# Performance work log

Hardware: AMD Instinct MI355X
Metric: run time of the kernel (lower is better)

The kernel has to match this reference:

```python
import jax, jax.numpy as jnp
import numpy as np

M_POOL = 12500  # rows of the down_transform sparse matrix


def setup_inputs() -> dict:
    key = jax.random.key(0)
    ks = jax.random.split(key, 6)
    B, N, E, Cin, Cout, K, P = 4, 50000, 800000, 32, 64, 6, 50000
    x = jax.random.normal(ks[0], (B, N, Cin), jnp.float32)
    edge_index = jax.random.randint(ks[1], (2, E), 0, N, dtype=jnp.int64)
    pool_row = jax.random.randint(ks[2], (P,), 0, M_POOL, dtype=jnp.int64)
    pool_col = jax.random.randint(ks[3], (P,), 0, N, dtype=jnp.int64)
    pool_val = jax.random.uniform(ks[4], (P,), jnp.float32)
    # xavier_uniform over each [Cin, Cout] slice; bias zero-init (reset_parameters)
    limit = np.sqrt(6.0 / (Cin + Cout)).astype(np.float32)
    weight = jax.random.uniform(ks[5], (K, Cin, Cout), jnp.float32, -limit, limit)
    bias = jnp.zeros((Cout,), jnp.float32)
    return dict(x=x, edge_index=edge_index, pool_row=pool_row,
                pool_col=pool_col, pool_val=pool_val, weight=weight, bias=bias)


def _cheb_conv(x, edge_index, weight, bias):
    # x: [B, N, Cin]; weight: [K, Cin, Cout]
    N = x.shape[1]
    row, col = edge_index[0], edge_index[1]
    ones = jnp.ones(row.shape, x.dtype)
    deg = jax.ops.segment_sum(ones, row, num_segments=N)
    dis = jnp.where(deg > 0, jax.lax.rsqrt(jnp.where(deg > 0, deg, 1.0)), 0.0)
    # L_hat = 2L/lambda_max - I with lambda_max=2, sym norm -> diag 0, off-diag -d_i^-1/2 d_j^-1/2
    norm = -dis[row] * dis[col]  # [E]

    def prop(h):  # h: [B, N, C] -> L_hat @ h (gather, scale, scatter_add)
        msgs = h[:, col, :] * norm[None, :, None]  # [B, E, C]
        return jnp.zeros_like(h).at[:, row, :].add(msgs)

    Tx0 = x
    out = jnp.einsum('bnc,co->bno', Tx0, weight[0])
    Tx1 = prop(Tx0)
    out = out + jnp.einsum('bnc,co->bno', Tx1, weight[1])
    for k in range(2, weight.shape[0]):
        Tx2 = 2.0 * prop(Tx1) - Tx0
        out = out + jnp.einsum('bnc,co->bno', Tx2, weight[k])
        Tx0, Tx1 = Tx1, Tx2
    return out + bias


def reference(x, edge_index, pool_row, pool_col, pool_val, weight, bias):
    h = _cheb_conv(x, edge_index, weight, bias)  # single block (n_blocks=1)
    h = jax.nn.elu(h)
    # Pool: gather columns, scale by sparse values, scatter_add into rows
    B, _, C = h.shape
    gathered = h[:, pool_col, :] * pool_val[None, :, None]  # [B, P, C]
    out = jnp.zeros((B, M_POOL, C), h.dtype).at[:, pool_row, :].add(gathered)
    return out
```

## Files before the change

### kernel.cpp

```cpp
#include <hip/hip_runtime.h>
#include <hip/hip_fp16.h>
#include <cstdint>

#define N_NODES 50000
#define B_SZ 4
#define C_IN 32
#define C_OUT 64
#define K_CHEB 6
#define M_POOL 12500
#define NT_ROWS (N_NODES + M_POOL)
#define NS32 ((size_t)N_NODES * C_IN)
#define ZH ((size_t)N_NODES * C_OUT)
#define CN_CAP 2048

typedef _Float16 f16x8 __attribute__((ext_vector_type(8)));
typedef float f32x4 __attribute__((ext_vector_type(4)));
typedef unsigned short ushort_t;

__device__ __forceinline__ unsigned short f2h(float f) {
    union { _Float16 h; unsigned short u; } v;
    v.h = (_Float16)f;
    return v.u;
}

__device__ __forceinline__ float h2f(unsigned short u) {
    union { unsigned short u; _Float16 h; } v;
    v.u = u;
    return (float)v.h;
}

__device__ __forceinline__ __half2 u2h2(unsigned u) { return __builtin_bit_cast(__half2, u); }
__device__ __forceinline__ unsigned h22u(__half2 h) { return __builtin_bit_cast(unsigned, h); }

__global__ void zero_deg_kernel(int* __restrict__ deg) {
    int i = blockIdx.x * 256 + threadIdx.x;
    if (i < NT_ROWS) deg[i] = 0;
}

__global__ void deg_slot_kernel(const int* __restrict__ row, const int* __restrict__ prow,
                                int* __restrict__ deg, int* __restrict__ slot, int E, int P) {
    int base = (blockIdx.x * blockDim.x + threadIdx.x) * 4;
#pragma unroll
    for (int k = 0; k < 4; k++) {
        int e = base + k;
        if (e < E) slot[e] = atomicAdd(&deg[row[e]], 1);
        else if (e < E + P) slot[e] = atomicAdd(&deg[N_NODES + prow[e - E]], 1);
    }
}

__global__ void disdegp_kernel(const int* __restrict__ deg, float* __restrict__ dis,
                               int* __restrict__ degp) {
    int i = blockIdx.x * blockDim.x + threadIdx.x;
    if (i < N_NODES) {
        int d = deg[i];
        dis[i] = d > 0 ? rsqrtf((float)d) : 0.f;
        degp[i] = (d + 3) & ~3;
    } else if (i < NT_ROWS) {
        degp[i] = deg[i];
    }
}

__global__ void block_sum_kernel(const int* __restrict__ degp, int* __restrict__ bsum, int N) {
    __shared__ int sm[256];
    int i = blockIdx.x * 256 + threadIdx.x;
    sm[threadIdx.x] = (i < N) ? degp[i] : 0;
    __syncthreads();
    for (int s = 128; s > 0; s >>= 1) {
        if (threadIdx.x < s) sm[threadIdx.x] += sm[threadIdx.x + s];
        __syncthreads();
    }
    if (threadIdx.x == 0) bsum[blockIdx.x] = sm[0];
}

__global__ void scan_bsum_kernel(int* bsum, int nb, int* rowptr, int N) {
    if (blockIdx.x == 0 && threadIdx.x == 0) {
        int run = 0;
        for (int i = 0; i < nb; i++) { int v = bsum[i]; bsum[i] = run; run += v; }
        rowptr[N] = run;
    }
}

__global__ void rowptr_kernel(const int* __restrict__ degp, const int* __restrict__ bsum,
                              int* __restrict__ rowptr, int N) {
    __shared__ int sm[256];
    int i = blockIdx.x * 256 + threadIdx.x;
    sm[threadIdx.x] = (i < N) ? degp[i] : 0;
    __syncthreads();
    if (threadIdx.x == 0) {
        int run = bsum[blockIdx.x];
        for (int t = 0; t < 256; t++) { int v = sm[t]; sm[t] = run; run += v; }
    }
    __syncthreads();
    if (i < N) rowptr[i] = sm[threadIdx.x];
}

__global__ void pad_fill_kernel(const int* __restrict__ deg, const int* __restrict__ rowptr,
                                int2* __restrict__ cn) {
    int r = blockIdx.x * blockDim.x + threadIdx.x;
    if (r >= N_NODES) return;
    int p = rowptr[r] + deg[r];
    int p1 = rowptr[r + 1];
    for (; p < p1; ++p) cn[p] = make_int2(0, 0);
}

__global__ void place_all_kernel(const int* __restrict__ row, const int* __restrict__ col,
                                 const int* __restrict__ prow, const int* __restrict__ pcol,
                                 const float* __restrict__ pval, const float* __restrict__ dis,
                                 const int* __restrict__ rowptr, const int* __restrict__ slot,
                                 int2* __restrict__ cn, int E, int P) {
    int e = blockIdx.x * blockDim.x + threadIdx.x;
    if (e < E) {
        int r = row[e], c = col[e];
        float nm = -dis[r] * dis[c];
        unsigned h = f2h(nm);
        cn[rowptr[r] + slot[e]] = make_int2(c, (int)(h | (h << 16)));
    } else if (e < E + P) {
        int i = e - E;
        int r = N_NODES + prow[i];
        cn[rowptr[r] + slot[e]] = make_int2(pcol[i], __float_as_int(pval[i]));
    }
}

__global__ void cast_h_kernel(const float* __restrict__ in, unsigned int* __restrict__ out,
                              int n2) {
    int i = blockIdx.x * 256 + threadIdx.x;
    if (i < n2) {
        unsigned a = f2h(in[2 * i]), b = f2h(in[2 * i + 1]);
        out[i] = a | (b << 16);
    }
}

__global__ void prop_kernel(const ushort_t* __restrict__ hf, const ushort_t* __restrict__ p2f,
                            ushort_t* __restrict__ outf,
                            const int* __restrict__ rowptr, const int2* __restrict__ cn,
                            float alpha) {
    __shared__ int2 lcn[CN_CAP];
    int bid = blockIdx.x;
    int b = bid & 3;
    int grp = bid >> 2;
    int r0 = grp * 64;
    int rend = r0 + 64 > N_NODES ? N_NODES : r0 + 64;
    int pbase = rowptr[r0];
    int pend = rowptr[rend];
    int cnt = pend - pbase;
    bool use_lds = (cnt <= CN_CAP);
    if (use_lds) {
        for (int i = threadIdx.x; i < cnt; i += 256) lcn[i] = cn[pbase + i];
    }
    __syncthreads();

    int lr = threadIdx.x >> 2;
    int cs = threadIdx.x & 3;
    int r = r0 + lr;
    if (r >= N_NODES) return;
    const char* hb = (const char*)hf + (size_t)b * NS32 * 2;
    unsigned coff = (unsigned)cs * 16u;
    __half2 a0 = __float2half2_rn(0.f), a1 = a0, a2 = a0, a3 = a0;

    if (use_lds) {
        int p0 = rowptr[r] - pbase, p1 = rowptr[r + 1] - pbase;
        for (int p = p0; p < p1; p += 4) {
            int2 e0 = lcn[p], e1 = lcn[p + 1], e2 = lcn[p + 2], e3 = lcn[p + 3];
            uint4 v0 = *(const uint4*)(hb + (((unsigned)e0.x << 6) + coff));
            uint4 v1 = *(const uint4*)(hb + (((unsigned)e1.x << 6) + coff));
            uint4 v2 = *(const uint4*)(hb + (((unsigned)e2.x << 6) + coff));
            uint4 v3 = *(const uint4*)(hb + (((unsigned)e3.x << 6) + coff));
            __half2 n0 = u2h2((unsigned)e0.y), n1 = u2h2((unsigned)e1.y);
            __half2 n2 = u2h2((unsigned)e2.y), n3 = u2h2((unsigned)e3.y);
            a0 = __hfma2(u2h2(v0.x), n0, a0); a1 = __hfma2(u2h2(v0.y), n0, a1);
            a2 = __hfma2(u2h2(v0.z), n0, a2); a3 = __hfma2(u2h2(v0.w), n0, a3);
            a0 = __hfma2(u2h2(v1.x), n1, a0); a1 = __hfma2(u2h2(v1.y), n1, a1);
            a2 = __hfma2(u2h2(v1.z), n1, a2); a3 = __hfma2(u2h2(v1.w), n1, a3);
            a0 = __hfma2(u2h2(v2.x), n2, a0); a1 = __hfma2(u2h2(v2.y), n2, a1);
            a2 = __hfma2(u2h2(v2.z), n2, a2); a3 = __hfma2(u2h2(v2.w), n2, a3);
            a0 = __hfma2(u2h2(v3.x), n3, a0); a1 = __hfma2(u2h2(v3.y), n3, a1);
            a2 = __hfma2(u2h2(v3.z), n3, a2); a3 = __hfma2(u2h2(v3.w), n3, a3);
        }
    } else {
        int p0 = rowptr[r], p1 = rowptr[r + 1];
        for (int p = p0; p < p1; p += 4) {
            int2 e0 = cn[p], e1 = cn[p + 1], e2 = cn[p + 2], e3 = cn[p + 3];
            uint4 v0 = *(const uint4*)(hb + (((unsigned)e0.x << 6) + coff));
            uint4 v1 = *(const uint4*)(hb + (((unsigned)e1.x << 6) + coff));
            uint4 v2 = *(const uint4*)(hb + (((unsigned)e2.x << 6) + coff));
            uint4 v3 = *(const uint4*)(hb + (((unsigned)e3.x << 6) + coff));
            __half2 n0 = u2h2((unsigned)e0.y), n1 = u2h2((unsigned)e1.y);
            __half2 n2 = u2h2((unsigned)e2.y), n3 = u2h2((unsigned)e3.y);
            a0 = __hfma2(u2h2(v0.x), n0, a0); a1 = __hfma2(u2h2(v0.y), n0, a1);
            a2 = __hfma2(u2h2(v0.z), n0, a2); a3 = __hfma2(u2h2(v0.w), n0, a3);
            a0 = __hfma2(u2h2(v1.x), n1, a0); a1 = __hfma2(u2h2(v1.y), n1, a1);
            a2 = __hfma2(u2h2(v1.z), n1, a2); a3 = __hfma2(u2h2(v1.w), n1, a3);
            a0 = __hfma2(u2h2(v2.x), n2, a0); a1 = __hfma2(u2h2(v2.y), n2, a1);
            a2 = __hfma2(u2h2(v2.z), n2, a2); a3 = __hfma2(u2h2(v2.w), n2, a3);
            a0 = __hfma2(u2h2(v3.x), n3, a0); a1 = __hfma2(u2h2(v3.y), n3, a1);
            a2 = __hfma2(u2h2(v3.z), n3, a2); a3 = __hfma2(u2h2(v3.w), n3, a3);
        }
    }

    unsigned ooff = ((unsigned)r << 6) + coff;
    uint4 o;
    if (p2f) {
        __half2 al2 = __float2half2_rn(alpha);
        uint4 pv = *(const uint4*)((const char*)p2f + (size_t)b * NS32 * 2 + ooff);
        o.x = h22u(__hfma2(a0, al2, __hneg2(u2h2(pv.x))));
        o.y = h22u(__hfma2(a1, al2, __hneg2(u2h2(pv.y))));
        o.z = h22u(__hfma2(a2, al2, __hneg2(u2h2(pv.z))));
        o.w = h22u(__hfma2(a3, al2, __hneg2(u2h2(pv.w))));
    } else {
        o.x = h22u(a0); o.y = h22u(a1); o.z = h22u(a2); o.w = h22u(a3);
    }
    *(uint4*)((char*)outf + (size_t)b * NS32 * 2 + ooff) = o;
}

__global__ void packW_kernel(const float* __restrict__ W, ushort_t* __restrict__ Wp) {
    int i = blockIdx.x * 256 + threadIdx.x;
    if (i >= K_CHEB * 4 * 64 * 8) return;
    int j = i & 7;
    int lane = (i >> 3) & 63;
    int t = (i >> 9) & 3;
    int s = i >> 11;
    int k = (lane >> 4) * 8 + j;
    int col = t * 16 + (lane & 15);
    Wp[i] = f2h(W[((size_t)s * C_IN + k) * C_OUT + col]);
}

__global__ void gemm_mfma_kernel(const ushort_t* __restrict__ T0, const ushort_t* __restrict__ T1,
                                 const ushort_t* __restrict__ T2, const ushort_t* __restrict__ T3,
                                 const ushort_t* __restrict__ T4, const ushort_t* __restrict__ T5,
                                 const ushort_t* __restrict__ Wp,
                                 const float* __restrict__ bias, ushort_t* __restrict__ z) {
    int lane = threadIdx.x & 63;
    int wave = (blockIdx.x << 2) + (threadIdx.x >> 6);
    int r0 = wave << 4;
    int ga = r0 + (lane & 15);
    int koff = (lane >> 4) * 8;
    const ushort_t* Ts[6] = {T0, T1, T2, T3, T4, T5};

    f16x8 afr[6];
#pragma unroll
    for (int s = 0; s < 6; s++)
        afr[s] = *(const f16x8*)(Ts[s] + (size_t)ga * C_IN + koff);

    int orow = r0 + ((lane >> 4) << 2);
#pragma unroll
    for (int t = 0; t < 4; t++) {
        f32x4 acc = {0.f, 0.f, 0.f, 0.f};
#pragma unroll
        for (int s = 0; s < 6; s++) {
            f16x8 bfr = *(const f16x8*)(Wp + ((s * 4 + t) * 64 + lane) * 8);
            acc = __builtin_amdgcn_mfma_f32_16x16x32_f16(afr[s], bfr, acc, 0, 0, 0);
        }
        int col = (t << 4) + (lane & 15);
        float bv = bias[col];
#pragma unroll
        for (int rg = 0; rg < 4; rg++) {
            float v = acc[rg] + bv;
            z[(size_t)(orow + rg) * C_OUT + col] = f2h(v > 0.f ? v : (expf(v) - 1.f));
        }
    }
}

__global__ void pool_csr_kernel(const ushort_t* __restrict__ z, const int* __restrict__ rowptr,
                                const int2* __restrict__ cn, float* __restrict__ out) {
    int r = blockIdx.x * 8 + (threadIdx.x >> 5);
    int c2 = threadIdx.x & 31;
    if (r >= M_POOL) return;
    const char* zb = (const char*)z;
    unsigned coff = (unsigned)c2 << 2;
    float s00 = 0.f, s01 = 0.f, s10 = 0.f, s11 = 0.f;
    float s20 = 0.f, s21 = 0.f, s30 = 0.f, s31 = 0.f;
    int p0 = rowptr[N_NODES + r], p1 = rowptr[N_NODES + r + 1];
    for (int p = p0; p < p1; ++p) {
        int2 e = cn[p];
        float v = __int_as_float(e.y);
        unsigned off = ((unsigned)e.x << 7) + coff;
        unsigned u0 = *(const unsigned*)(zb + off);
        unsigned u1 = *(const unsigned*)(zb + ZH * 2 + off);
        unsigned u2 = *(const unsigned*)(zb + 2 * ZH * 2 + off);
        unsigned u3 = *(const unsigned*)(zb + 3 * ZH * 2 + off);
        s00 += h2f((ushort_t)u0) * v; s01 += h2f((ushort_t)(u0 >> 16)) * v;
        s10 += h2f((ushort_t)u1) * v; s11 += h2f((ushort_t)(u1 >> 16)) * v;
        s20 += h2f((ushort_t)u2) * v; s21 += h2f((ushort_t)(u2 >> 16)) * v;
        s30 += h2f((ushort_t)u3) * v; s31 += h2f((ushort_t)(u3 >> 16)) * v;
    }
    size_t idx = (size_t)r * C_OUT + 2 * c2;
    size_t bs = (size_t)M_POOL * C_OUT;
    *(float2*)&out[idx]          = make_float2(s00, s01);
    *(float2*)&out[idx + bs]     = make_float2(s10, s11);
    *(float2*)&out[idx + 2 * bs] = make_float2(s20, s21);
    *(float2*)&out[idx + 3 * bs] = make_float2(s30, s31);
}

extern "C" void kernel_launch(void* const* d_in, const int* in_sizes, int n_in,
                              void* d_out, int out_size, void* d_ws, size_t ws_size,
                              hipStream_t stream) {
    const float* x    = (const float*)d_in[0];
    const int*   ei   = (const int*)d_in[1];
    const int*   prow = (const int*)d_in[2];
    const int*   pcol = (const int*)d_in[3];
    const float* pval = (const float*)d_in[4];
    const float* W    = (const float*)d_in[5];
    const float* bias = (const float*)d_in[6];
    const int E = in_sizes[1] / 2;
    const int P = in_sizes[2];
    const int* row = ei;
    const int* col = ei + E;
    const int EP_MAX = E + 3 * N_NODES + P;

    char* ws = (char*)d_ws;
    size_t o = 0;
    auto alloc = [&](size_t bytes) -> char* {
        char* p = ws + o;
        o += (bytes + 255) & ~(size_t)255;
        return p;
    };
    int nb = (NT_ROWS + 255) / 256;
    int*   deg    = (int*)alloc((size_t)NT_ROWS * 4);
    int*   degp   = (int*)alloc((size_t)NT_ROWS * 4);
    float* dis    = (float*)alloc((size_t)N_NODES * 4);
    int*   rowptr = (int*)alloc((size_t)(NT_ROWS + 1) * 4);
    int*   slot   = (int*)alloc((size_t)(E + P) * 4);
    int*   bsum   = (int*)alloc((size_t)nb * 4);
    int2*  cn     = (int2*)alloc((size_t)EP_MAX * 8);
    ushort_t* Wp  = (ushort_t*)alloc((size_t)K_CHEB * 4 * 64 * 8 * 2);
    ushort_t* xh  = (ushort_t*)alloc((size_t)B_SZ * NS32 * 2);
    ushort_t* hA  = (ushort_t*)alloc((size_t)B_SZ * NS32 * 2);
    ushort_t* hB  = (ushort_t*)alloc((size_t)B_SZ * NS32 * 2);
    ushort_t* hC  = (ushort_t*)alloc((size_t)B_SZ * NS32 * 2);
    ushort_t* hD  = (ushort_t*)alloc((size_t)B_SZ * NS32 * 2);
    ushort_t* hE  = (ushort_t*)alloc((size_t)B_SZ * NS32 * 2);
    ushort_t* z   = (ushort_t*)alloc((size_t)B_SZ * ZH * 2);

    zero_deg_kernel<<<nb, 256, 0, stream>>>(deg);
    deg_slot_kernel<<<(E + P + 1023) / 1024, 256, 0, stream>>>(row, prow, deg, slot, E, P);
    disdegp_kernel<<<nb, 256, 0, stream>>>(deg, dis, degp);
    block_sum_kernel<<<nb, 256, 0, stream>>>(degp, bsum, NT_ROWS);
    scan_bsum_kernel<<<1, 64, 0, stream>>>(bsum, nb, rowptr, NT_ROWS);
    rowptr_kernel<<<nb, 256, 0, stream>>>(degp, bsum, rowptr, NT_ROWS);
    pad_fill_kernel<<<(N_NODES + 255) / 256, 256, 0, stream>>>(deg, rowptr, cn);
    place_all_kernel<<<(E + P + 255) / 256, 256, 0, stream>>>(row, col, prow, pcol, pval, dis,
                                                              rowptr, slot, cn, E, P);
    packW_kernel<<<(K_CHEB * 4 * 64 * 8 + 255) / 256, 256, 0, stream>>>(W, Wp);
    int n2 = (int)(B_SZ * NS32 / 2);
    cast_h_kernel<<<(n2 + 255) / 256, 256, 0, stream>>>(x, (unsigned int*)xh, n2);

    int prop_blocks = ((N_NODES + 63) / 64) * B_SZ;
    int gemm_blocks = (B_SZ * N_NODES) / 64;

    prop_kernel<<<prop_blocks, 256, 0, stream>>>(xh, nullptr, hA, rowptr, cn, 1.0f);
    prop_kernel<<<prop_blocks, 256, 0, stream>>>(hA, xh, hB, rowptr, cn, 2.0f);
    prop_kernel<<<prop_blocks, 256, 0, stream>>>(hB, hA, hC, rowptr, cn, 2.0f);
    prop_kernel<<<prop_blocks, 256, 0, stream>>>(hC, hB, hD, rowptr, cn, 2.0f);
    prop_kernel<<<prop_blocks, 256, 0, stream>>>(hD, hC, hE, rowptr, cn, 2.0f);
    gemm_mfma_kernel<<<gemm_blocks, 256, 0, stream>>>(xh, hA, hB, hC, hD, hE, Wp, bias, z);
    pool_csr_kernel<<<(M_POOL + 7) / 8, 256, 0, stream>>>(z, rowptr, cn, (float*)d_out);
}
```

Before: 269.7 us.

## Pad CSR rows to 8, unroll gather by 8, parallelize scan and pool per batch

Pads each graph row's neighbor list to a multiple of 8 and unrolls the propagation gather loop to 8 independent loads, so more memory requests are in flight. The block-sum scan becomes a parallel Hillis-Steele scan in shared memory instead of a single-thread loop. The pool kernel is split across batches to launch more blocks, and the degree kernel handles one edge per thread. Wider padding adds more zero-weight entries and gathers of padded slots, plus more registers per thread.

```diff
diff --git a/kernel.cpp b/kernel.cpp
--- a/kernel.cpp
+++ b/kernel.cpp
@@ -39,13 +39,9 @@
 
 __global__ void deg_slot_kernel(const int* __restrict__ row, const int* __restrict__ prow,
                                 int* __restrict__ deg, int* __restrict__ slot, int E, int P) {
-    int base = (blockIdx.x * blockDim.x + threadIdx.x) * 4;
-#pragma unroll
-    for (int k = 0; k < 4; k++) {
-        int e = base + k;
-        if (e < E) slot[e] = atomicAdd(&deg[row[e]], 1);
-        else if (e < E + P) slot[e] = atomicAdd(&deg[N_NODES + prow[e - E]], 1);
-    }
+    int e = blockIdx.x * blockDim.x + threadIdx.x;
+    if (e < E) slot[e] = atomicAdd(&deg[row[e]], 1);
+    else if (e < E + P) slot[e] = atomicAdd(&deg[N_NODES + prow[e - E]], 1);
 }
 
 __global__ void disdegp_kernel(const int* __restrict__ deg, float* __restrict__ dis,
@@ -54,7 +50,7 @@
     if (i < N_NODES) {
         int d = deg[i];
         dis[i] = d > 0 ? rsqrtf((float)d) : 0.f;
-        degp[i] = (d + 3) & ~3;
+        degp[i] = (d + 7) & ~7;
     } else if (i < NT_ROWS) {
         degp[i] = deg[i];
     }
@@ -73,11 +69,19 @@
 }
 
 __global__ void scan_bsum_kernel(int* bsum, int nb, int* rowptr, int N) {
-    if (blockIdx.x == 0 && threadIdx.x == 0) {
-        int run = 0;
-        for (int i = 0; i < nb; i++) { int v = bsum[i]; bsum[i] = run; run += v; }
-        rowptr[N] = run;
-    }
+    __shared__ int sm[256];
+    int t = threadIdx.x;
+    int v = (t < nb) ? bsum[t] : 0;
+    sm[t] = v;
+    __syncthreads();
+    for (int off = 1; off < 256; off <<= 1) {
+        int u = (t >= off) ? sm[t - off] : 0;
+        __syncthreads();
+        sm[t] += u;
+        __syncthreads();
+    }
+    if (t < nb) bsum[t] = sm[t] - v;
+    if (t == 0) rowptr[N] = sm[255];
 }
 
 __global__ void rowptr_kernel(const int* __restrict__ degp, const int* __restrict__ bsum,
@@ -159,41 +163,41 @@
 
     if (use_lds) {
         int p0 = rowptr[r] - pbase, p1 = rowptr[r + 1] - pbase;
-        for (int p = p0; p < p1; p += 4) {
-            int2 e0 = lcn[p], e1 = lcn[p + 1], e2 = lcn[p + 2], e3 = lcn[p + 3];
-            uint4 v0 = *(const uint4*)(hb + (((unsigned)e0.x << 6) + coff));
-            uint4 v1 = *(const uint4*)(hb + (((unsigned)e1.x << 6) + coff));
-            uint4 v2 = *(const uint4*)(hb + (((unsigned)e2.x << 6) + coff));
-            uint4 v3 = *(const uint4*)(hb + (((unsigned)e3.x << 6) + coff));
-            __half2 n0 = u2h2((unsigned)e0.y), n1 = u2h2((unsigned)e1.y);
-            __half2 n2 = u2h2((unsigned)e2.y), n3 = u2h2((unsigned)e3.y);
-            a0 = __hfma2(u2h2(v0.x), n0, a0); a1 = __hfma2(u2h2(v0.y), n0, a1);
-            a2 = __hfma2(u2h2(v0.z), n0, a2); a3 = __hfma2(u2h2(v0.w), n0, a3);
-            a0 = __hfma2(u2h2(v1.x), n1, a0); a1 = __hfma2(u2h2(v1.y), n1, a1);
-            a2 = __hfma2(u2h2(v1.z), n1, a2); a3 = __hfma2(u2h2(v1.w), n1, a3);
-            a0 = __hfma2(u2h2(v2.x), n2, a0); a1 = __hfma2(u2h2(v2.y), n2, a1);
-            a2 = __hfma2(u2h2(v2.z), n2, a2); a3 = __hfma2(u2h2(v2.w), n2, a3);
-            a0 = __hfma2(u2h2(v3.x), n3, a0); a1 = __hfma2(u2h2(v3.y), n3, a1);
-            a2 = __hfma2(u2h2(v3.z), n3, a2); a3 = __hfma2(u2h2(v3.w), n3, a3);
+        for (int p = p0; p < p1; p += 8) {
+            int2 ea[8];
+#pragma unroll
+            for (int i = 0; i < 8; i++) ea[i] = lcn[p + i];
+            uint4 v[8];
+#pragma unroll
+            for (int i = 0; i < 8; i++)
+                v[i] = *(const uint4*)(hb + (((unsigned)ea[i].x << 6) + coff));
+#pragma unroll
+            for (int i = 0; i < 8; i++) {
+                __half2 n = u2h2((unsigned)ea[i].y);
+                a0 = __hfma2(u2h2(v[i].x), n, a0);
+                a1 = __hfma2(u2h2(v[i].y), n, a1);
+                a2 = __hfma2(u2h2(v[i].z), n, a2);
+                a3 = __hfma2(u2h2(v[i].w), n, a3);
+            }
         }
     } else {
         int p0 = rowptr[r], p1 = rowptr[r + 1];
-        for (int p = p0; p < p1; p += 4) {
-            int2 e0 = cn[p], e1 = cn[p + 1], e2 = cn[p + 2], e3 = cn[p + 3];
-            uint4 v0 = *(const uint4*)(hb + (((unsigned)e0.x << 6) + coff));
-            uint4 v1 = *(const uint4*)(hb + (((unsigned)e1.x << 6) + coff));
-            uint4 v2 = *(const uint4*)(hb + (((unsigned)e2.x << 6) + coff));
-            uint4 v3 = *(const uint4*)(hb + (((unsigned)e3.x << 6) + coff));
-            __half2 n0 = u2h2((unsigned)e0.y), n1 = u2h2((unsigned)e1.y);
-            __half2 n2 = u2h2((unsigned)e2.y), n3 = u2h2((unsigned)e3.y);
-            a0 = __hfma2(u2h2(v0.x), n0, a0); a1 = __hfma2(u2h2(v0.y), n0, a1);
-            a2 = __hfma2(u2h2(v0.z), n0, a2); a3 = __hfma2(u2h2(v0.w), n0, a3);
-            a0 = __hfma2(u2h2(v1.x), n1, a0); a1 = __hfma2(u2h2(v1.y), n1, a1);
-            a2 = __hfma2(u2h2(v1.z), n1, a2); a3 = __hfma2(u2h2(v1.w), n1, a3);
-            a0 = __hfma2(u2h2(v2.x), n2, a0); a1 = __hfma2(u2h2(v2.y), n2, a1);
-            a2 = __hfma2(u2h2(v2.z), n2, a2); a3 = __hfma2(u2h2(v2.w), n2, a3);
-            a0 = __hfma2(u2h2(v3.x), n3, a0); a1 = __hfma2(u2h2(v3.y), n3, a1);
-            a2 = __hfma2(u2h2(v3.z), n3, a2); a3 = __hfma2(u2h2(v3.w), n3, a3);
+        for (int p = p0; p < p1; p += 8) {
+            int2 ea[8];
+#pragma unroll
+            for (int i = 0; i < 8; i++) ea[i] = cn[p + i];
+            uint4 v[8];
+#pragma unroll
+            for (int i = 0; i < 8; i++)
+                v[i] = *(const uint4*)(hb + (((unsigned)ea[i].x << 6) + coff));
+#pragma unroll
+            for (int i = 0; i < 8; i++) {
+                __half2 n = u2h2((unsigned)ea[i].y);
+                a0 = __hfma2(u2h2(v[i].x), n, a0);
+                a1 = __hfma2(u2h2(v[i].y), n, a1);
+                a2 = __hfma2(u2h2(v[i].z), n, a2);
+                a3 = __hfma2(u2h2(v[i].w), n, a3);
+            }
         }
     }
 
@@ -262,33 +266,24 @@
 
 __global__ void pool_csr_kernel(const ushort_t* __restrict__ z, const int* __restrict__ rowptr,
                                 const int2* __restrict__ cn, float* __restrict__ out) {
-    int r = blockIdx.x * 8 + (threadIdx.x >> 5);
+    int bid = blockIdx.x;
+    int b = bid & 3;
+    int r = (bid >> 2) * 8 + (threadIdx.x >> 5);
     int c2 = threadIdx.x & 31;
     if (r >= M_POOL) return;
-    const char* zb = (const char*)z;
+    const char* zb = (const char*)z + (size_t)b * ZH * 2;
     unsigned coff = (unsigned)c2 << 2;
-    float s00 = 0.f, s01 = 0.f, s10 = 0.f, s11 = 0.f;
-    float s20 = 0.f, s21 = 0.f, s30 = 0.f, s31 = 0.f;
+    float s0 = 0.f, s1 = 0.f;
     int p0 = rowptr[N_NODES + r], p1 = rowptr[N_NODES + r + 1];
     for (int p = p0; p < p1; ++p) {
         int2 e = cn[p];
         float v = __int_as_float(e.y);
-        unsigned off = ((unsigned)e.x << 7) + coff;
-        unsigned u0 = *(const unsigned*)(zb + off);
-        unsigned u1 = *(const unsigned*)(zb + ZH * 2 + off);
-        unsigned u2 = *(const unsigned*)(zb + 2 * ZH * 2 + off);
-        unsigned u3 = *(const unsigned*)(zb + 3 * ZH * 2 + off);
-        s00 += h2f((ushort_t)u0) * v; s01 += h2f((ushort_t)(u0 >> 16)) * v;
-        s10 += h2f((ushort_t)u1) * v; s11 += h2f((ushort_t)(u1 >> 16)) * v;
-        s20 += h2f((ushort_t)u2) * v; s21 += h2f((ushort_t)(u2 >> 16)) * v;
-        s30 += h2f((ushort_t)u3) * v; s31 += h2f((ushort_t)(u3 >> 16)) * v;
-    }
-    size_t idx = (size_t)r * C_OUT + 2 * c2;
-    size_t bs = (size_t)M_POOL * C_OUT;
-    *(float2*)&out[idx]          = make_float2(s00, s01);
-    *(float2*)&out[idx + bs]     = make_float2(s10, s11);
-    *(float2*)&out[idx + 2 * bs] = make_float2(s20, s21);
-    *(float2*)&out[idx + 3 * bs] = make_float2(s30, s31);
+        unsigned u = *(const unsigned*)(zb + (((unsigned)e.x << 7) + coff));
+        s0 += h2f((ushort_t)u) * v;
+        s1 += h2f((ushort_t)(u >> 16)) * v;
+    }
+    size_t idx = (size_t)b * M_POOL * C_OUT + (size_t)r * C_OUT + 2 * c2;
+    *(float2*)&out[idx] = make_float2(s0, s1);
 }
 
 extern "C" void kernel_launch(void* const* d_in, const int* in_sizes, int n_in,
@@ -305,7 +300,7 @@
     const int P = in_sizes[2];
     const int* row = ei;
     const int* col = ei + E;
-    const int EP_MAX = E + 3 * N_NODES + P;
+    const int EP_MAX = E + 7 * N_NODES + P;
 
     char* ws = (char*)d_ws;
     size_t o = 0;
@@ -332,10 +327,10 @@
     ushort_t* z   = (ushort_t*)alloc((size_t)B_SZ * ZH * 2);
 
     zero_deg_kernel<<<nb, 256, 0, stream>>>(deg);
-    deg_slot_kernel<<<(E + P + 1023) / 1024, 256, 0, stream>>>(row, prow, deg, slot, E, P);
+    deg_slot_kernel<<<(E + P + 255) / 256, 256, 0, stream>>>(row, prow, deg, slot, E, P);
     disdegp_kernel<<<nb, 256, 0, stream>>>(deg, dis, degp);
     block_sum_kernel<<<nb, 256, 0, stream>>>(degp, bsum, NT_ROWS);
-    scan_bsum_kernel<<<1, 64, 0, stream>>>(bsum, nb, rowptr, NT_ROWS);
+    scan_bsum_kernel<<<1, 256, 0, stream>>>(bsum, nb, rowptr, NT_ROWS);
     rowptr_kernel<<<nb, 256, 0, stream>>>(degp, bsum, rowptr, NT_ROWS);
     pad_fill_kernel<<<(N_NODES + 255) / 256, 256, 0, stream>>>(deg, rowptr, cn);
     place_all_kernel<<<(E + P + 255) / 256, 256, 0, stream>>>(row, col, prow, pcol, pval, dis,
@@ -353,5 +348,6 @@
     prop_kernel<<<prop_blocks, 256, 0, stream>>>(hC, hB, hD, rowptr, cn, 2.0f);
     prop_kernel<<<prop_blocks, 256, 0, stream>>>(hD, hC, hE, rowptr, cn, 2.0f);
     gemm_mfma_kernel<<<gemm_blocks, 256, 0, stream>>>(xh, hA, hB, hC, hD, hE, Wp, bias, z);
-    pool_csr_kernel<<<(M_POOL + 7) / 8, 256, 0, stream>>>(z, rowptr, cn, (float*)d_out);
-}
+    pool_csr_kernel<<<((M_POOL + 7) / 8) * B_SZ, 256, 0, stream>>>(z, rowptr, cn,
+                                                                   (float*)d_out);
+}
```

Result: faster. 255.6 us (-5.2%).
